# Kernel optimization log

Hardware: AMD Instinct MI355X
Metric: run time of the kernel (lower is better)

The kernel has to match this reference:

```python
import jax, jax.numpy as jnp
import numpy as np

N_NODES = 100000
N_EDGES = 3200000
IN_F, HID, OUT = 24, 64, 1


def _gcn_conv(x, W, b, src, dst, norm, n):
    # x: [N, Fin] -> h: [N, Fout]; PyG GCNConv: lin first, then normalized aggregation, then bias
    h = x @ W                                    # [N, Fout]
    msg = h[src] * norm[:, None]                 # [E+N, Fout] gathered, norm-weighted messages
    agg = jax.ops.segment_sum(msg, dst, num_segments=n)  # scatter-add to targets
    return agg + b


def setup_inputs() -> dict:
    key = jax.random.key(0)
    k1, k2, k3, k4 = jax.random.split(key, 4)
    x = jax.random.normal(k1, (N_NODES, IN_F), dtype=jnp.float32)
    edge_index = jax.random.randint(k2, (2, N_EDGES), 0, N_NODES, dtype=jnp.int64)
    # Glorot-ish init for weights
    W1 = jax.random.normal(k3, (IN_F, HID), dtype=jnp.float32) / np.sqrt(IN_F)
    b1 = jnp.zeros((HID,), dtype=jnp.float32)
    W2 = jax.random.normal(k4, (HID, OUT), dtype=jnp.float32) / np.sqrt(HID)
    b2 = jnp.zeros((OUT,), dtype=jnp.float32)
    return {"x": x, "edge_index": edge_index, "W1": W1, "b1": b1, "W2": W2, "b2": b2}


def reference(x, edge_index, W1, b1, W2, b2):
    n = x.shape[0]
    # add self-loops (PyG GCNConv default)
    loops = jnp.arange(n, dtype=edge_index.dtype)
    src = jnp.concatenate([edge_index[0], loops])
    dst = jnp.concatenate([edge_index[1], loops])
    # symmetric normalization: deg over targets of A+I, norm_e = d^-1/2[src] * d^-1/2[dst]
    deg = jax.ops.segment_sum(jnp.ones_like(dst, dtype=x.dtype), dst, num_segments=n)
    dinv = jnp.where(deg > 0, jax.lax.rsqrt(deg), 0.0)
    norm = dinv[src] * dinv[dst]
    h = _gcn_conv(x, W1, b1, src, dst, norm, n)
    h = jax.nn.relu(h)
    # F.dropout with training=self.training -> identity in eval mode (reference runs eval)
    out = _gcn_conv(h, W2, b2, src, dst, norm, n)
    return out
```

## Files before the change

kernel.cpp:

```cpp
#include <hip/hip_runtime.h>
#include <hip/hip_fp16.h>

#define IN_F 24
#define HID 64
#define NB 512
#define NPB 256
#define GSZ_MAX 256
#define PBUF 7168
#define SRC_BITS 17

typedef unsigned int u32;

__device__ __forceinline__ int bucket_lo(int b, int n) {
    return (int)(((long long)b * n + NB - 1) / NB);
}

__global__ __launch_bounds__(256) void k_pcount(const int* __restrict__ dst,
                                                u32* __restrict__ pc, int e, int n) {
    __shared__ u32 h[NB];
    for (int j = threadIdx.x; j < NB; j += 256) h[j] = 0;
    __syncthreads();
    int blk = blockIdx.x;
    long long begin = (long long)e * blk / NPB;
    long long end   = (long long)e * (blk + 1) / NPB;
    for (long long i = begin + threadIdx.x; i < end; i += 256) {
        int k = (int)((long long)dst[i] * NB / n);
        atomicAdd(&h[k], 1u);
    }
    __syncthreads();
    for (int j = threadIdx.x; j < NB; j += 256) pc[(size_t)blk * NB + j] = h[j];
}

__global__ __launch_bounds__(256) void k_pscan_a(u32* __restrict__ pc,
                                                 u32* __restrict__ colsum) {
    __shared__ u32 ps[256];
    int t = blockIdx.x;
    int tid = threadIdx.x;
    u32 v = pc[(size_t)tid * NB + t];
    ps[tid] = v;
    __syncthreads();
    for (int off = 1; off < 256; off <<= 1) {
        u32 v2 = (tid >= off) ? ps[tid - off] : 0;
        __syncthreads();
        ps[tid] += v2;
        __syncthreads();
    }
    pc[(size_t)tid * NB + t] = ps[tid] - v;
    if (tid == 255) colsum[t] = ps[255];
}

__global__ void k_pscan_b(const u32* __restrict__ colsum, u32* __restrict__ basep) {
    __shared__ u32 s[NB];
    int t = threadIdx.x;
    u32 v = colsum[t];
    s[t] = v;
    __syncthreads();
    for (int off = 1; off < NB; off <<= 1) {
        u32 v2 = (t >= off) ? s[t - off] : 0;
        __syncthreads();
        s[t] += v2;
        __syncthreads();
    }
    basep[t] = s[t] - v;
}

__global__ __launch_bounds__(256) void k_part(const int* __restrict__ src,
                                              const int* __restrict__ dst,
                                              const u32* __restrict__ pc,
                                              const u32* __restrict__ basep,
                                              u32* __restrict__ pairs, int e, int n) {
    __shared__ u32 cur[NB];
    int blk = (blockIdx.x & 7) * (NPB / 8) + (blockIdx.x >> 3);
    for (int j = threadIdx.x; j < NB; j += 256)
        cur[j] = pc[(size_t)blk * NB + j] + basep[j];
    __syncthreads();
    long long begin = (long long)e * blk / NPB;
    long long end   = (long long)e * (blk + 1) / NPB;
    for (long long i = begin + threadIdx.x; i < end; i += 256) {
        int d = dst[i];
        int sv = src[i];
        int k = (int)((long long)d * NB / n);
        u32 loc = (u32)(d - bucket_lo(k, n));
        u32 pos = atomicAdd(&cur[k], 1u);
        pairs[pos] = (loc << SRC_BITS) | (u32)sv;
    }
}

__global__ __launch_bounds__(256) void k_bucket(const u32* __restrict__ pairs,
                                                const u32* __restrict__ basep,
                                                const float* __restrict__ x,
                                                int* __restrict__ cnt,
                                                int* __restrict__ row_start,
                                                float* __restrict__ dinv,
                                                int* __restrict__ csr_src,
                                                __half2* __restrict__ xs2, int e, int n) {
    __shared__ u32 pbuf[PBUF];
    __shared__ u32 h[GSZ_MAX];
    __shared__ u32 cur[GSZ_MAX];
    __shared__ u32 sc[GSZ_MAX];
    __shared__ float dloc[GSZ_MAX];
    int b = blockIdx.x;
    int lo = bucket_lo(b, n);
    int hi = bucket_lo(b + 1, n);
    int gsz = hi - lo;
    u32 start = basep[b];
    u32 endp = (b + 1 < NB) ? basep[b + 1] : (u32)e;
    int nbp = (int)(endp - start);
    for (int j = threadIdx.x; j < GSZ_MAX; j += 256) h[j] = 0;
    __syncthreads();
    int stored = nbp < PBUF ? nbp : PBUF;
    for (int i = threadIdx.x; i < stored; i += 256) {
        u32 p = pairs[start + i];
        pbuf[i] = p;
        atomicAdd(&h[p >> SRC_BITS], 1u);
    }
    for (int i = PBUF + threadIdx.x; i < nbp; i += 256) {
        atomicAdd(&h[pairs[start + i] >> SRC_BITS], 1u);
    }
    __syncthreads();
    int t = threadIdx.x;
    u32 v = h[t];
    sc[t] = v;
    __syncthreads();
    for (int off = 1; off < 256; off <<= 1) {
        u32 v2 = (t >= off) ? sc[t - off] : 0;
        __syncthreads();
        sc[t] += v2;
        __syncthreads();
    }
    u32 excl = sc[t] - v;
    if (t < gsz) {
        float dv = rsqrtf((float)(v + 1));
        cnt[lo + t] = (int)v;
        row_start[lo + t] = (int)(start + excl);
        dinv[lo + t] = dv;
        dloc[t] = dv;
        cur[t] = excl;
    }
    __syncthreads();
    for (int i = threadIdx.x; i < stored; i += 256) {
        u32 p = pbuf[i];
        u32 pos = atomicAdd(&cur[p >> SRC_BITS], 1u);
        csr_src[start + pos] = (int)(p & ((1u << SRC_BITS) - 1));
    }
    for (int i = PBUF + threadIdx.x; i < nbp; i += 256) {
        u32 p = pairs[start + i];
        u32 pos = atomicAdd(&cur[p >> SRC_BITS], 1u);
        csr_src[start + pos] = (int)(p & ((1u << SRC_BITS) - 1));
    }
    const float2* xf = (const float2*)(x + (long long)lo * IN_F);
    for (int i = threadIdx.x; i < gsz * 12; i += 256) {
        float2 vv = xf[i];
        float dn = dloc[i / 12];
        xs2[(long long)lo * 12 + i] = __floats2half2_rn(vv.x * dn, vv.y * dn);
    }
}

__global__ void k_agg1(const float* __restrict__ x, const __half2* __restrict__ xs2,
                       const float* __restrict__ dinv, const int* __restrict__ row_start,
                       const int* __restrict__ cnt, const int* __restrict__ csr_src,
                       float2* __restrict__ aggX2, int n) {
    int t = blockIdx.x * blockDim.x + threadIdx.x;
    int node = t >> 4;
    int f2 = t & 15;
    if (node >= n || f2 >= 12) return;
    int row = row_start[node];
    int c = cnt[node];
    float ax = 0.0f, ay = 0.0f;
    int j = 0;
    for (; j + 8 <= c; j += 8) {
        const int* cp = csr_src + row + j;
        int s0 = cp[0], s1 = cp[1], s2 = cp[2], s3 = cp[3];
        int s4 = cp[4], s5 = cp[5], s6 = cp[6], s7 = cp[7];
        __half2 h0 = xs2[s0 * 12 + f2];
        __half2 h1 = xs2[s1 * 12 + f2];
        __half2 h2 = xs2[s2 * 12 + f2];
        __half2 h3 = xs2[s3 * 12 + f2];
        __half2 h4 = xs2[s4 * 12 + f2];
        __half2 h5 = xs2[s5 * 12 + f2];
        __half2 h6 = xs2[s6 * 12 + f2];
        __half2 h7 = xs2[s7 * 12 + f2];
        float2 f0 = __half22float2(h0), f1 = __half22float2(h1);
        float2 f2v = __half22float2(h2), f3 = __half22float2(h3);
        float2 f4 = __half22float2(h4), f5 = __half22float2(h5);
        float2 f6 = __half22float2(h6), f7 = __half22float2(h7);
        ax += (f0.x + f1.x) + (f2v.x + f3.x) + ((f4.x + f5.x) + (f6.x + f7.x));
        ay += (f0.y + f1.y) + (f2v.y + f3.y) + ((f4.y + f5.y) + (f6.y + f7.y));
    }
    for (; j < c; ++j) {
        int s = csr_src[row + j];
        float2 fv = __half22float2(xs2[s * 12 + f2]);
        ax += fv.x;
        ay += fv.y;
    }
    float dn = dinv[node];
    float sx = x[(long long)node * IN_F + 2 * f2];
    float sy = x[(long long)node * IN_F + 2 * f2 + 1];
    float2 outv;
    outv.x = (ax + sx * dn) * dn;
    outv.y = (ay + sy * dn) * dn;
    aggX2[(long long)node * 12 + f2] = outv;
}

__global__ __launch_bounds__(256) void k_hidden_z(const float* __restrict__ aggX,
                                                  const float* __restrict__ W1,
                                                  const float* __restrict__ b1,
                                                  const float* __restrict__ W2,
                                                  const float* __restrict__ dinv,
                                                  float* __restrict__ zs, int n) {
    __shared__ float w[IN_F * HID];
    __shared__ float w2s[HID];
    __shared__ float b1s[HID];
    for (int j = threadIdx.x; j < IN_F * HID; j += 256) w[j] = W1[j];
    if (threadIdx.x < HID) { w2s[threadIdx.x] = W2[threadIdx.x]; b1s[threadIdx.x] = b1[threadIdx.x]; }
    __syncthreads();
    int node = blockIdx.x * 256 + threadIdx.x;
    if (node >= n) return;
    float h[HID];
#pragma unroll
    for (int f = 0; f < HID; ++f) h[f] = b1s[f];
    const float4* xp = (const float4*)(aggX + (long long)node * IN_F);
#pragma unroll
    for (int kk = 0; kk < IN_F / 4; ++kk) {
        float4 xv = xp[kk];
        const float* w0 = w + (kk * 4) * HID;
#pragma unroll
        for (int f = 0; f < HID; ++f) h[f] += xv.x * w0[f];
        const float* w1r = w0 + HID;
#pragma unroll
        for (int f = 0; f < HID; ++f) h[f] += xv.y * w1r[f];
        const float* w2r = w1r + HID;
#pragma unroll
        for (int f = 0; f < HID; ++f) h[f] += xv.z * w2r[f];
        const float* w3r = w2r + HID;
#pragma unroll
        for (int f = 0; f < HID; ++f) h[f] += xv.w * w3r[f];
    }
    float acc = 0.0f;
#pragma unroll
    for (int f = 0; f < HID; ++f) acc += fmaxf(h[f], 0.0f) * w2s[f];
    zs[node] = acc * dinv[node];
}

__global__ void k_out(const float* __restrict__ zs, const float* __restrict__ dinv,
                      const int* __restrict__ row_start, const int* __restrict__ cnt,
                      const int* __restrict__ csr_src, const float* __restrict__ b2,
                      float* __restrict__ out, int n) {
    int t = blockIdx.x * blockDim.x + threadIdx.x;
    int node = t >> 4;
    int lane = t & 15;
    if (node >= n) return;
    int row = row_start[node];
    int c = cnt[node];
    float v = 0.0f;
    for (int j = lane; j < c; j += 16) {
        v += zs[csr_src[row + j]];
    }
    v += __shfl_down(v, 8, 16);
    v += __shfl_down(v, 4, 16);
    v += __shfl_down(v, 2, 16);
    v += __shfl_down(v, 1, 16);
    if (lane == 0) {
        out[node] = b2[0] + dinv[node] * (zs[node] + v);
    }
}

extern "C" void kernel_launch(void* const* d_in, const int* in_sizes, int n_in,
                              void* d_out, int out_size, void* d_ws, size_t ws_size,
                              hipStream_t stream) {
    const float* x   = (const float*)d_in[0];
    const int*   ei  = (const int*)d_in[1];
    const float* W1  = (const float*)d_in[2];
    const float* b1  = (const float*)d_in[3];
    const float* W2  = (const float*)d_in[4];
    const float* b2  = (const float*)d_in[5];
    float* out = (float*)d_out;

    const int n = in_sizes[0] / IN_F;
    const int e = in_sizes[1] / 2;
    const int* src = ei;
    const int* dst = ei + e;

    const int B = 256;

    char* base = (char*)d_ws;
    u32* pairs     = (u32*)base;
    float* aggX    = (float*)base;
    float* zs      = aggX + (size_t)n * IN_F;
    size_t ov = (size_t)e * 4;
    size_t ov2 = (size_t)n * 100;
    if (ov2 > ov) ov = ov2;
    ov = (ov + 255) & ~(size_t)255;
    char* after    = base + ov;
    int* cnt       = (int*)after;
    int* row_start = cnt + n;
    int* csr_src   = row_start + n;
    float* dinv    = (float*)(csr_src + e);
    __half* xs     = (__half*)(dinv + n);
    u32* pc        = (u32*)(xs + (size_t)n * IN_F);
    u32* colsum    = pc + (size_t)NPB * NB;
    u32* basep     = colsum + NB;

    k_pcount<<<NPB, B, 0, stream>>>(dst, pc, e, n);
    k_pscan_a<<<NB, B, 0, stream>>>(pc, colsum);
    k_pscan_b<<<1, NB, 0, stream>>>(colsum, basep);
    k_part<<<NPB, B, 0, stream>>>(src, dst, pc, basep, pairs, e, n);
    k_bucket<<<NB, B, 0, stream>>>(pairs, basep, x, cnt, row_start, dinv, csr_src,
                                   (__half2*)xs, e, n);

    const long long n16 = (long long)n * 16;
    k_agg1<<<(int)((n16 + B - 1) / B), B, 0, stream>>>(x, (const __half2*)xs, dinv,
                                                      row_start, cnt, csr_src,
                                                      (float2*)aggX, n);
    k_hidden_z<<<(n + B - 1) / B, B, 0, stream>>>(aggX, W1, b1, W2, dinv, zs, n);

    k_out<<<(int)((n16 + B - 1) / B), B, 0, stream>>>(zs, dinv, row_start, cnt, csr_src, b2, out, n);
}
```

Measured before the change: 227.0 us.

## Fuse first-layer aggregation with hidden transform and output projection

Merges the layer-1 neighbor aggregation kernel and the per-node hidden/z kernel into one kernel. Aggregated features stay in shared memory instead of making a global round trip through an aggX buffer. The 64-wide hidden computation is split across 16 lanes per node, with 4 features each and a shuffle reduction, replacing the old one-thread-per-node loop that held 64 registers. Each block now loads W1 into shared memory but covers only 16 nodes, which adds redundant weight loads per block and an extra barrier.

```diff
diff --git a/kernel.cpp b/kernel.cpp
--- a/kernel.cpp
+++ b/kernel.cpp
@@ -156,90 +156,83 @@
     }
 }
 
-__global__ void k_agg1(const float* __restrict__ x, const __half2* __restrict__ xs2,
-                       const float* __restrict__ dinv, const int* __restrict__ row_start,
-                       const int* __restrict__ cnt, const int* __restrict__ csr_src,
-                       float2* __restrict__ aggX2, int n) {
-    int t = blockIdx.x * blockDim.x + threadIdx.x;
-    int node = t >> 4;
-    int f2 = t & 15;
-    if (node >= n || f2 >= 12) return;
-    int row = row_start[node];
-    int c = cnt[node];
-    float ax = 0.0f, ay = 0.0f;
-    int j = 0;
-    for (; j + 8 <= c; j += 8) {
-        const int* cp = csr_src + row + j;
-        int s0 = cp[0], s1 = cp[1], s2 = cp[2], s3 = cp[3];
-        int s4 = cp[4], s5 = cp[5], s6 = cp[6], s7 = cp[7];
-        __half2 h0 = xs2[s0 * 12 + f2];
-        __half2 h1 = xs2[s1 * 12 + f2];
-        __half2 h2 = xs2[s2 * 12 + f2];
-        __half2 h3 = xs2[s3 * 12 + f2];
-        __half2 h4 = xs2[s4 * 12 + f2];
-        __half2 h5 = xs2[s5 * 12 + f2];
-        __half2 h6 = xs2[s6 * 12 + f2];
-        __half2 h7 = xs2[s7 * 12 + f2];
-        float2 f0 = __half22float2(h0), f1 = __half22float2(h1);
-        float2 f2v = __half22float2(h2), f3 = __half22float2(h3);
-        float2 f4 = __half22float2(h4), f5 = __half22float2(h5);
-        float2 f6 = __half22float2(h6), f7 = __half22float2(h7);
-        ax += (f0.x + f1.x) + (f2v.x + f3.x) + ((f4.x + f5.x) + (f6.x + f7.x));
-        ay += (f0.y + f1.y) + (f2v.y + f3.y) + ((f4.y + f5.y) + (f6.y + f7.y));
-    }
-    for (; j < c; ++j) {
-        int s = csr_src[row + j];
-        float2 fv = __half22float2(xs2[s * 12 + f2]);
-        ax += fv.x;
-        ay += fv.y;
-    }
-    float dn = dinv[node];
-    float sx = x[(long long)node * IN_F + 2 * f2];
-    float sy = x[(long long)node * IN_F + 2 * f2 + 1];
-    float2 outv;
-    outv.x = (ax + sx * dn) * dn;
-    outv.y = (ay + sy * dn) * dn;
-    aggX2[(long long)node * 12 + f2] = outv;
-}
-
-__global__ __launch_bounds__(256) void k_hidden_z(const float* __restrict__ aggX,
-                                                  const float* __restrict__ W1,
-                                                  const float* __restrict__ b1,
-                                                  const float* __restrict__ W2,
-                                                  const float* __restrict__ dinv,
-                                                  float* __restrict__ zs, int n) {
+__global__ __launch_bounds__(256) void k_agg_hz(const float* __restrict__ x,
+                                                const __half2* __restrict__ xs2,
+                                                const float* __restrict__ dinv,
+                                                const int* __restrict__ row_start,
+                                                const int* __restrict__ cnt,
+                                                const int* __restrict__ csr_src,
+                                                const float* __restrict__ W1,
+                                                const float* __restrict__ b1,
+                                                const float* __restrict__ W2,
+                                                float* __restrict__ zs, int n) {
     __shared__ float w[IN_F * HID];
     __shared__ float w2s[HID];
     __shared__ float b1s[HID];
+    __shared__ float sagg[16][25];
     for (int j = threadIdx.x; j < IN_F * HID; j += 256) w[j] = W1[j];
     if (threadIdx.x < HID) { w2s[threadIdx.x] = W2[threadIdx.x]; b1s[threadIdx.x] = b1[threadIdx.x]; }
-    __syncthreads();
-    int node = blockIdx.x * 256 + threadIdx.x;
-    if (node >= n) return;
-    float h[HID];
+    int g = threadIdx.x >> 4;
+    int f2 = threadIdx.x & 15;
+    int node = blockIdx.x * 16 + g;
+    __syncthreads();
+    if (node < n && f2 < 12) {
+        int row = row_start[node];
+        int c = cnt[node];
+        float ax = 0.0f, ay = 0.0f;
+        int j = 0;
+        for (; j + 8 <= c; j += 8) {
+            const int* cp = csr_src + row + j;
+            int s0 = cp[0], s1 = cp[1], s2 = cp[2], s3 = cp[3];
+            int s4 = cp[4], s5 = cp[5], s6 = cp[6], s7 = cp[7];
+            __half2 h0 = xs2[s0 * 12 + f2];
+            __half2 h1 = xs2[s1 * 12 + f2];
+            __half2 h2 = xs2[s2 * 12 + f2];
+            __half2 h3 = xs2[s3 * 12 + f2];
+            __half2 h4 = xs2[s4 * 12 + f2];
+            __half2 h5 = xs2[s5 * 12 + f2];
+            __half2 h6 = xs2[s6 * 12 + f2];
+            __half2 h7 = xs2[s7 * 12 + f2];
+            float2 f0 = __half22float2(h0), f1 = __half22float2(h1);
+            float2 f2v = __half22float2(h2), f3 = __half22float2(h3);
+            float2 f4 = __half22float2(h4), f5 = __half22float2(h5);
+            float2 f6 = __half22float2(h6), f7 = __half22float2(h7);
+            ax += (f0.x + f1.x) + (f2v.x + f3.x) + ((f4.x + f5.x) + (f6.x + f7.x));
+            ay += (f0.y + f1.y) + (f2v.y + f3.y) + ((f4.y + f5.y) + (f6.y + f7.y));
+        }
+        for (; j < c; ++j) {
+            int s = csr_src[row + j];
+            float2 fv = __half22float2(xs2[s * 12 + f2]);
+            ax += fv.x;
+            ay += fv.y;
+        }
+        float dn = dinv[node];
+        float sx = x[(long long)node * IN_F + 2 * f2];
+        float sy = x[(long long)node * IN_F + 2 * f2 + 1];
+        sagg[g][2 * f2]     = (ax + sx * dn) * dn;
+        sagg[g][2 * f2 + 1] = (ay + sy * dn) * dn;
+    }
+    __syncthreads();
+    if (node < n) {
+        int fb = f2 * 4;
+        float h0 = b1s[fb], h1 = b1s[fb + 1], h2 = b1s[fb + 2], h3 = b1s[fb + 3];
 #pragma unroll
-    for (int f = 0; f < HID; ++f) h[f] = b1s[f];
-    const float4* xp = (const float4*)(aggX + (long long)node * IN_F);
-#pragma unroll
-    for (int kk = 0; kk < IN_F / 4; ++kk) {
-        float4 xv = xp[kk];
-        const float* w0 = w + (kk * 4) * HID;
-#pragma unroll
-        for (int f = 0; f < HID; ++f) h[f] += xv.x * w0[f];
-        const float* w1r = w0 + HID;
-#pragma unroll
-        for (int f = 0; f < HID; ++f) h[f] += xv.y * w1r[f];
-        const float* w2r = w1r + HID;
-#pragma unroll
-        for (int f = 0; f < HID; ++f) h[f] += xv.z * w2r[f];
-        const float* w3r = w2r + HID;
-#pragma unroll
-        for (int f = 0; f < HID; ++f) h[f] += xv.w * w3r[f];
-    }
-    float acc = 0.0f;
-#pragma unroll
-    for (int f = 0; f < HID; ++f) acc += fmaxf(h[f], 0.0f) * w2s[f];
-    zs[node] = acc * dinv[node];
+        for (int k = 0; k < IN_F; ++k) {
+            float xv = sagg[g][k];
+            const float* wr = w + k * HID + fb;
+            h0 += xv * wr[0];
+            h1 += xv * wr[1];
+            h2 += xv * wr[2];
+            h3 += xv * wr[3];
+        }
+        float p = fmaxf(h0, 0.0f) * w2s[fb] + fmaxf(h1, 0.0f) * w2s[fb + 1]
+                + fmaxf(h2, 0.0f) * w2s[fb + 2] + fmaxf(h3, 0.0f) * w2s[fb + 3];
+        p += __shfl_down(p, 8, 16);
+        p += __shfl_down(p, 4, 16);
+        p += __shfl_down(p, 2, 16);
+        p += __shfl_down(p, 1, 16);
+        if (f2 == 0) zs[node] = p * dinv[node];
+    }
 }
 
 __global__ void k_out(const float* __restrict__ zs, const float* __restrict__ dinv,
@@ -285,12 +278,8 @@
 
     char* base = (char*)d_ws;
     u32* pairs     = (u32*)base;
-    float* aggX    = (float*)base;
-    float* zs      = aggX + (size_t)n * IN_F;
-    size_t ov = (size_t)e * 4;
-    size_t ov2 = (size_t)n * 100;
-    if (ov2 > ov) ov = ov2;
-    ov = (ov + 255) & ~(size_t)255;
+    float* zs      = (float*)base;
+    size_t ov = ((size_t)e * 4 + 255) & ~(size_t)255;
     char* after    = base + ov;
     int* cnt       = (int*)after;
     int* row_start = cnt + n;
@@ -308,11 +297,10 @@
     k_bucket<<<NB, B, 0, stream>>>(pairs, basep, x, cnt, row_start, dinv, csr_src,
                                    (__half2*)xs, e, n);
 
+    k_agg_hz<<<(n + 15) / 16, B, 0, stream>>>(x, (const __half2*)xs, dinv,
+                                              row_start, cnt, csr_src,
+                                              W1, b1, W2, zs, n);
+
     const long long n16 = (long long)n * 16;
-    k_agg1<<<(int)((n16 + B - 1) / B), B, 0, stream>>>(x, (const __half2*)xs, dinv,
-                                                      row_start, cnt, csr_src,
-                                                      (float2*)aggX, n);
-    k_hidden_z<<<(n + B - 1) / B, B, 0, stream>>>(aggX, W1, b1, W2, dinv, zs, n);
-
     k_out<<<(int)((n16 + B - 1) / B), B, 0, stream>>>(zs, dinv, row_start, cnt, csr_src, b2, out, n);
 }
```

New measurement: 223.5 us. No clear change (-1.5%).
